# Optimization experiments

Measured on AMD Instinct MI355X. Metric: run time of the kernel, lower is better.

Reference implementation:

```python
import jax, jax.numpy as jnp
import numpy as np

B, T, DIM, FF, E, TOPK = 2, 2048, 1024, 4096, 8, 2


def setup_inputs() -> dict:
    key = jax.random.key(0)
    k0, k1, k2, k3 = jax.random.split(key, 4)
    x = jax.random.normal(k0, (B, T, DIM), jnp.float32)
    # router weight [E, D] (nn.Linear(dim, num_experts, bias=False))
    Wr = jax.random.normal(k1, (E, DIM), jnp.float32) * (DIM ** -0.5)
    # per-expert FFN weights, stacked: W1 [E, D, FF], W2 [E, FF, D]
    W1 = jax.random.normal(k2, (E, DIM, FF), jnp.float32) * (DIM ** -0.5)
    W2 = jax.random.normal(k3, (E, FF, DIM), jnp.float32) * (FF ** -0.5)
    return {"x": x, "Wr": Wr, "W1": W1, "W2": W2}


def reference(x, Wr, W1, W2):
    """MoEFeedForward.forward, world_size=1, STANDARD implementation.

    Math: per token, top_k experts by router logits, softmax over the top_k
    logits (fp32), y = sum_k w_k * FFN_{e_k}(x). The torch code realizes this
    via sort/permute + per-expert variable-size GEMM + weighted index_add;
    the scatter-add result is identical to the dense masked form below,
    which is the jit-friendly (static-shape) expression.
    """
    Bn, Tn, D = x.shape
    num_experts = Wr.shape[0]
    xf = x.reshape(-1, D)                      # [N, D], N = B*T
    N = xf.shape[0]

    logits = xf @ Wr.T                         # [N, E]
    topw, topi = jax.lax.top_k(logits, TOPK)   # [N, K]
    topw = jax.nn.softmax(topw.astype(jnp.float32), axis=-1).astype(x.dtype)

    # combine weight for each (token, expert): [N, E] (0 if not routed)
    combine = jnp.zeros((N, num_experts), x.dtype)
    combine = combine.at[jnp.arange(N)[:, None], topi].add(topw)

    out = jnp.zeros_like(xf)
    for e in range(num_experts):               # fixed small loop over experts
        h = jax.nn.gelu(xf @ W1[e], approximate=False)  # exact GELU (nn.GELU)
        out = out + combine[:, e:e + 1] * (h @ W2[e])
    return out.reshape(Bn, Tn, D)
```

## Files before the change

kernel.cpp:

```cpp
#include <hip/hip_runtime.h>
#include <hip/hip_bf16.h>
#include <hip/hip_fp16.h>

#define NTOK 4096
#define DIM 1024
#define FF 4096
#define NE 8
#define NSLOT 8192

typedef _Float16 half8 __attribute__((ext_vector_type(8)));
typedef _Float16 half4 __attribute__((ext_vector_type(4)));
typedef float floatx4 __attribute__((ext_vector_type(4)));

__device__ __forceinline__ float gelu_exact(float x) {
    return 0.5f * x * (1.0f + erff(x * 0.70710678118654752f));
}

__device__ __forceinline__ void gl_lds16(const void* g, void* l) {
    __builtin_amdgcn_global_load_lds(
        (const __attribute__((address_space(1))) void*)g,
        (__attribute__((address_space(3))) void*)l, 16, 0, 0);
}

__global__ __launch_bounds__(256) void k_convert_x(const float* __restrict__ x,
                                                   _Float16* __restrict__ xh) {
    int i = (blockIdx.x * 256 + threadIdx.x) * 8;
    float4 a = *(const float4*)(x + i);
    float4 b = *(const float4*)(x + i + 4);
    half8 h;
    h[0] = (_Float16)a.x; h[1] = (_Float16)a.y; h[2] = (_Float16)a.z; h[3] = (_Float16)a.w;
    h[4] = (_Float16)b.x; h[5] = (_Float16)b.y; h[6] = (_Float16)b.z; h[7] = (_Float16)b.w;
    *(half8*)(xh + i) = h;
}

__global__ __launch_bounds__(256) void k_transpose(const float* __restrict__ src,
                                                   _Float16* __restrict__ dst,
                                                   int R, int C) {
    __shared__ float t[64][65];
    int e = blockIdx.z;
    const float* s = src + (size_t)e * R * C;
    _Float16* d = dst + (size_t)e * C * R;
    int r0 = blockIdx.y * 64, c0 = blockIdx.x * 64;
    int tid = threadIdx.x;
    int rr = tid >> 4, cc = (tid & 15) * 4;
#pragma unroll
    for (int i = 0; i < 4; ++i) {
        float4 v = *(const float4*)(s + (size_t)(r0 + rr + i * 16) * C + c0 + cc);
        t[rr + i * 16][cc] = v.x; t[rr + i * 16][cc + 1] = v.y;
        t[rr + i * 16][cc + 2] = v.z; t[rr + i * 16][cc + 3] = v.w;
    }
    __syncthreads();
    int f = tid >> 3, ch = tid & 7;
#pragma unroll
    for (int j = 0; j < 2; ++j) {
        int fr = f + j * 32;
        half8 v;
#pragma unroll
        for (int u = 0; u < 8; ++u) v[u] = (_Float16)t[ch * 8 + u][fr];
        *(half8*)(d + (size_t)(c0 + fr) * R + r0 + ch * 8) = v;
    }
}

__global__ __launch_bounds__(256) void k_router(const float* __restrict__ x,
                                                const float* __restrict__ Wr,
                                                int* __restrict__ counts,
                                                int* __restrict__ tok_e,
                                                float* __restrict__ tok_w,
                                                int* __restrict__ tok_pos) {
    __shared__ float wr[NE * DIM];
    int tid = threadIdx.x;
    for (int i = tid; i < NE * DIM / 4; i += 256)
        ((float4*)wr)[i] = ((const float4*)Wr)[i];
    __syncthreads();

    int w = tid >> 6, lane = tid & 63;
    int t = blockIdx.x * 4 + w;

    float acc[NE] = {};
    for (int j = 0; j < DIM / 64; ++j) {
        float xv = x[t * DIM + j * 64 + lane];
#pragma unroll
        for (int e = 0; e < NE; ++e)
            acc[e] += xv * wr[e * DIM + j * 64 + lane];
    }
#pragma unroll
    for (int e = 0; e < NE; ++e) {
#pragma unroll
        for (int s = 32; s; s >>= 1) acc[e] += __shfl_xor(acc[e], s, 64);
    }
    if (lane == 0) {
        int b0 = 0; float m0 = acc[0];
#pragma unroll
        for (int e = 1; e < NE; ++e) { if (acc[e] > m0) { m0 = acc[e]; b0 = e; } }
        int b1 = -1; float m1 = -1e30f;
#pragma unroll
        for (int e = 0; e < NE; ++e) { if (e != b0 && acc[e] > m1) { m1 = acc[e]; b1 = e; } }
        float z = __expf(m1 - m0);
        float zz = 1.0f / (1.0f + z);
        int p0 = atomicAdd(&counts[b0], 1);
        int p1 = atomicAdd(&counts[b1], 1);
        tok_e[2 * t] = b0;  tok_e[2 * t + 1] = b1;
        tok_w[2 * t] = zz;  tok_w[2 * t + 1] = z * zz;
        tok_pos[2 * t] = p0; tok_pos[2 * t + 1] = p1;
    }
}

__global__ void k_prefix(const int* __restrict__ counts, int* __restrict__ offs,
                         int* __restrict__ tmap256, int* __restrict__ tmap128) {
    if (threadIdx.x == 0 && blockIdx.x == 0) {
        int s = 0, n2 = 0, n1 = 0;
        for (int e = 0; e < NE; ++e) {
            offs[e] = s;
            int c = counts[e];
            for (int mt = 0; mt * 256 < c; ++mt) tmap256[1 + n2++] = (e << 16) | mt;
            for (int mt = 0; mt * 128 < c; ++mt) tmap128[1 + n1++] = (e << 16) | mt;
            s += c;
        }
        offs[NE] = s;
        tmap256[0] = n2;
        tmap128[0] = n1;
    }
}

__global__ __launch_bounds__(256) void k_slots(const int* __restrict__ offs,
                                               const int* __restrict__ tok_e,
                                               const int* __restrict__ tok_pos,
                                               int* __restrict__ tok_slot,
                                               int* __restrict__ list_tok) {
    int idx = blockIdx.x * 256 + threadIdx.x;
    if (idx < NSLOT) {
        int e = tok_e[idx];
        int slot = offs[e] + tok_pos[idx];
        tok_slot[idx] = slot;
        list_tok[slot] = idx >> 1;
    }
}

template<int K, int NOUT, int KSPAN, bool GATHER, bool GELU>
__global__ __launch_bounds__(512, 2) void k_ffn256(
    const _Float16* __restrict__ Abase,
    const _Float16* __restrict__ Wbase,
    const int* __restrict__ tmap,
    const int* __restrict__ counts,
    const int* __restrict__ offs,
    const int* __restrict__ list_tok,
    _Float16* __restrict__ Out) {

    int nt_m = tmap[0];
    if ((int)blockIdx.x >= nt_m) return;
    int ent = tmap[1 + blockIdx.x];
    int e = ent >> 16, mt = ent & 0xffff;
    int base = offs[e] + mt * 256;
    int valid = counts[e] - mt * 256;
    int f0 = blockIdx.y * 256;
    int kbase = blockIdx.z * KSPAN;
    Out += (size_t)blockIdx.z * ((size_t)NSLOT * NOUT);

    __shared__ _Float16 lds[65536];

    int tid = threadIdx.x;
    int wid = tid >> 6, lane = tid & 63;

    const char* AB = (const char*)Abase;
    const char* WB = (const char*)(Wbase + (size_t)e * NOUT * K);

    size_t aoff[4]; unsigned boff[4];
#pragma unroll
    for (int i = 0; i < 4; ++i) {
        int g = i * 512 + tid;
        int r = g >> 3;
        int c = (g & 7) ^ (r & 7);
        int rr = (r < valid) ? r : (valid - 1);
        unsigned arow = GATHER ? (unsigned)list_tok[base + rr] : (unsigned)(base + rr);
        aoff[i] = (size_t)arow * (K * 2) + c * 16 + (size_t)kbase * 2;
        boff[i] = (unsigned)(f0 + r) * (unsigned)(K * 2) + c * 16 + (unsigned)kbase * 2;
    }

    floatx4 acc[8][4];
#pragma unroll
    for (int m = 0; m < 8; ++m)
#pragma unroll
        for (int n = 0; n < 4; ++n) acc[m][n] = (floatx4){0.f, 0.f, 0.f, 0.f};

    int la = lane & 15, lb = lane >> 4;
    int wmb = (wid >> 2) * 128, wnb = (wid & 3) * 64;

#pragma unroll
    for (int i = 0; i < 4; ++i)
        gl_lds16(AB + aoff[i], lds + i * 4096 + wid * 512);
#pragma unroll
    for (int i = 0; i < 4; ++i)
        gl_lds16(WB + boff[i], lds + 32768 + i * 4096 + wid * 512);
    asm volatile("s_waitcnt vmcnt(0)" ::: "memory");
    __builtin_amdgcn_s_barrier();
    __builtin_amdgcn_sched_barrier(0);

    constexpr int NT = KSPAN / 64;
#pragma unroll 2
    for (int t = 0; t < NT; ++t) {
        int cur = t & 1;
        if (t + 1 < NT) {
            size_t adv = (size_t)(t + 1) * 128;
            _Float16* Ad = lds + (cur ^ 1) * 16384;
            _Float16* Bd = lds + 32768 + (cur ^ 1) * 16384;
#pragma unroll
            for (int i = 0; i < 4; ++i)
                gl_lds16(AB + aoff[i] + adv, Ad + i * 4096 + wid * 512);
#pragma unroll
            for (int i = 0; i < 4; ++i)
                gl_lds16(WB + boff[i] + adv, Bd + i * 4096 + wid * 512);
        }
        const _Float16* Ac = lds + cur * 16384;
        const _Float16* Bc = lds + 32768 + cur * 16384;
#pragma unroll
        for (int kk = 0; kk < 2; ++kk) {
            half8 af[8], bf[4];
#pragma unroll
            for (int n = 0; n < 4; ++n) {
                int row = wnb + n * 16 + la;
                int c = kk * 4 + lb;
                bf[n] = *(const half8*)(Bc + row * 64 + ((c ^ (row & 7)) * 8));
            }
#pragma unroll
            for (int m = 0; m < 8; ++m) {
                int row = wmb + m * 16 + la;
                int c = kk * 4 + lb;
                af[m] = *(const half8*)(Ac + row * 64 + ((c ^ (row & 7)) * 8));
            }
#pragma unroll
            for (int m = 0; m < 8; ++m)
#pragma unroll
                for (int n = 0; n < 4; ++n)
                    acc[m][n] = __builtin_amdgcn_mfma_f32_16x16x32_f16(af[m], bf[n], acc[m][n], 0, 0, 0);
        }
        __builtin_amdgcn_sched_barrier(0);
        asm volatile("s_waitcnt vmcnt(0)" ::: "memory");
        __builtin_amdgcn_s_barrier();
        __builtin_amdgcn_sched_barrier(0);
    }

    _Float16* tw = lds + wid * 4096;
#pragma unroll
    for (int ps = 0; ps < 2; ++ps) {
#pragma unroll
        for (int fi = 0; fi < 4; ++fi)
#pragma unroll
            for (int nf = 0; nf < 4; ++nf) {
                floatx4 v = acc[ps * 4 + fi][nf];
#pragma unroll
                for (int i2 = 0; i2 < 4; ++i2) {
                    float fv = v[i2];
                    if (GELU) fv = gelu_exact(fv);
                    tw[(fi * 16 + lb * 4 + i2) * 64 + nf * 16 + la] = (_Float16)fv;
                }
            }
        asm volatile("s_waitcnt lgkmcnt(0)" ::: "memory");
        __builtin_amdgcn_sched_barrier(0);
#pragma unroll
        for (int i2 = 0; i2 < 8; ++i2) {
            int gi = i2 * 64 + lane;
            int row = gi >> 3, c8 = gi & 7;
            half8 v = *(const half8*)(tw + gi * 8);
            int trow = wmb + ps * 64 + row;
            if (trow < valid)
                *(half8*)(Out + (size_t)(base + trow) * NOUT + f0 + wnb + c8 * 8) = v;
        }
    }
}

template<int K, int NOUT, bool GATHER, bool GELU>
__global__ __launch_bounds__(256) void k_ffn(
    const _Float16* __restrict__ Abase,
    const _Float16* __restrict__ Wbase,
    const int* __restrict__ tmap,
    const int* __restrict__ counts,
    const int* __restrict__ offs,
    const int* __restrict__ list_tok,
    _Float16* __restrict__ Out) {

    int nt_m = tmap[0];
    if ((int)blockIdx.x >= nt_m) return;
    int ent = tmap[1 + blockIdx.x];
    int e = ent >> 16, mt = ent & 0xffff;
    int base = offs[e] + mt * 128;
    int valid = counts[e] - mt * 128;
    int f0 = blockIdx.y * 128;

    __shared__ _Float16 lds[32768];

    int tid = threadIdx.x;
    int wid = tid >> 6, lane = tid & 63;

    const char* AB = (const char*)Abase;
    const char* WB = (const char*)(Wbase + (size_t)e * NOUT * K);

    size_t aoff[4]; unsigned boff[4];
#pragma unroll
    for (int i = 0; i < 4; ++i) {
        int g = wid * 256 + i * 64 + lane;
        int r = g >> 3;
        int c = (g & 7) ^ (r & 7);
        int rr = (r < valid) ? r : (valid - 1);
        unsigned arow = GATHER ? (unsigned)list_tok[base + rr] : (unsigned)(base + rr);
        aoff[i] = (size_t)arow * (K * 2) + c * 16;
        boff[i] = (unsigned)(f0 + r) * (unsigned)(K * 2) + c * 16;
    }

    floatx4 acc[4][4];
#pragma unroll
    for (int m = 0; m < 4; ++m)
#pragma unroll
        for (int n = 0; n < 4; ++n) acc[m][n] = (floatx4){0.f, 0.f, 0.f, 0.f};

    int la = lane & 15, lb = lane >> 4;
    int wm = (wid >> 1) * 64, wn = (wid & 1) * 64;

#pragma unroll
    for (int i = 0; i < 4; ++i)
        gl_lds16(AB + aoff[i], lds + wid * 2048 + i * 512);
#pragma unroll
    for (int i = 0; i < 4; ++i)
        gl_lds16(WB + boff[i], lds + 16384 + wid * 2048 + i * 512);
    asm volatile("s_waitcnt vmcnt(0)" ::: "memory");
    __builtin_amdgcn_s_barrier();
    __builtin_amdgcn_sched_barrier(0);

    constexpr int NT = K / 64;
#pragma unroll 2
    for (int t = 0; t < NT; ++t) {
        int cur = t & 1;
        if (t + 1 < NT) {
            size_t kadv = (size_t)(t + 1) * 128;
            _Float16* Ad = lds + (cur ^ 1) * 8192;
            _Float16* Bd = lds + 16384 + (cur ^ 1) * 8192;
#pragma unroll
            for (int i = 0; i < 4; ++i)
                gl_lds16(AB + aoff[i] + kadv, Ad + wid * 2048 + i * 512);
#pragma unroll
            for (int i = 0; i < 4; ++i)
                gl_lds16(WB + boff[i] + kadv, Bd + wid * 2048 + i * 512);
        }
        const _Float16* Ac = lds + cur * 8192;
        const _Float16* Bc = lds + 16384 + cur * 8192;
#pragma unroll
        for (int kk = 0; kk < 2; ++kk) {
            half8 af[4], bf[4];
#pragma unroll
            for (int m = 0; m < 4; ++m) {
                int row = wm + m * 16 + la;
                int c = kk * 4 + lb;
                af[m] = *(const half8*)(Ac + row * 64 + ((c ^ (row & 7)) * 8));
            }
#pragma unroll
            for (int n = 0; n < 4; ++n) {
                int row = wn + n * 16 + la;
                int c = kk * 4 + lb;
                bf[n] = *(const half8*)(Bc + row * 64 + ((c ^ (row & 7)) * 8));
            }
#pragma unroll
            for (int m = 0; m < 4; ++m)
#pragma unroll
                for (int n = 0; n < 4; ++n)
                    acc[m][n] = __builtin_amdgcn_mfma_f32_16x16x32_f16(af[m], bf[n], acc[m][n], 0, 0, 0);
        }
        __builtin_amdgcn_sched_barrier(0);
        asm volatile("s_waitcnt vmcnt(0)" ::: "memory");
        __builtin_amdgcn_s_barrier();
        __builtin_amdgcn_sched_barrier(0);
    }

    _Float16* tw = lds + wid * 4096;
#pragma unroll
    for (int m = 0; m < 4; ++m)
#pragma unroll
        for (int n = 0; n < 4; ++n) {
            floatx4 v = acc[m][n];
#pragma unroll
            for (int i = 0; i < 4; ++i) {
                float fv = v[i];
                if (GELU) fv = gelu_exact(fv);
                tw[(m * 16 + lb * 4 + i) * 64 + n * 16 + la] = (_Float16)fv;
            }
        }
    asm volatile("s_waitcnt lgkmcnt(0)" ::: "memory");
    __builtin_amdgcn_sched_barrier(0);
#pragma unroll
    for (int i = 0; i < 8; ++i) {
        int gi = i * 64 + lane;
        int row = gi >> 3, c8 = gi & 7;
        half8 v = *(const half8*)(tw + gi * 8);
        int trow = wm + row;
        if (trow < valid)
            *(half8*)(Out + (size_t)(base + trow) * NOUT + f0 + wn + c8 * 8) = v;
    }
}

__global__ __launch_bounds__(256) void k_combine(const _Float16* __restrict__ yp,
                                                 const int* __restrict__ tok_slot,
                                                 const float* __restrict__ tok_w,
                                                 float* __restrict__ out,
                                                 int nsplit) {
    int t = blockIdx.x;
    int d = threadIdx.x * 4;
    int s0 = tok_slot[2 * t], s1 = tok_slot[2 * t + 1];
    float w0 = tok_w[2 * t], w1 = tok_w[2 * t + 1];
    float4 sum0 = {0.f, 0.f, 0.f, 0.f}, sum1 = {0.f, 0.f, 0.f, 0.f};
    for (int z = 0; z < nsplit; ++z) {
        const _Float16* p = yp + (size_t)z * NSLOT * DIM;
        half4 y0 = *(const half4*)(p + (size_t)s0 * DIM + d);
        half4 y1 = *(const half4*)(p + (size_t)s1 * DIM + d);
        sum0.x += (float)y0[0]; sum0.y += (float)y0[1];
        sum0.z += (float)y0[2]; sum0.w += (float)y0[3];
        sum1.x += (float)y1[0]; sum1.y += (float)y1[1];
        sum1.z += (float)y1[2]; sum1.w += (float)y1[3];
    }
    float4 o;
    o.x = w0 * sum0.x + w1 * sum1.x;
    o.y = w0 * sum0.y + w1 * sum1.y;
    o.z = w0 * sum0.z + w1 * sum1.z;
    o.w = w0 * sum0.w + w1 * sum1.w;
    *(float4*)(out + (size_t)t * DIM + d) = o;
}

extern "C" void kernel_launch(void* const* d_in, const int* in_sizes, int n_in,
                              void* d_out, int out_size, void* d_ws, size_t ws_size,
                              hipStream_t stream) {
    const float* x  = (const float*)d_in[0];
    const float* Wr = (const float*)d_in[1];
    const float* W1 = (const float*)d_in[2];
    const float* W2 = (const float*)d_in[3];
    float* out = (float*)d_out;

    char* ws = (char*)d_ws;
    _Float16* w1t  = (_Float16*)ws;
    _Float16* w2t  = (_Float16*)ws;
    _Float16* xh   = (_Float16*)(ws + 67108864);
    _Float16* hbuf = (_Float16*)(ws + 75497472);
    char* p = ws + 142606336;
    int*   counts   = (int*)p;        p += 1024;
    int*   offs     = (int*)p;        p += 1024;
    int*   tmap256  = (int*)p;        p += 1024;
    int*   tmap128  = (int*)p;        p += 1024;
    int*   tok_e    = (int*)p;        p += NSLOT * 4;
    float* tok_w    = (float*)p;      p += NSLOT * 4;
    int*   tok_pos  = (int*)p;        p += NSLOT * 4;
    int*   tok_slot = (int*)p;        p += NSLOT * 4;
    int*   list_tok = (int*)p;        p += NSLOT * 4;
    const size_t OFF_Y = 142606336 + 196608;
    const size_t SZ_Y  = (size_t)NSLOT * DIM * 2;
    _Float16* yp = (_Float16*)(ws + OFF_Y);

    int nsplit = (ws_size >= OFF_Y + 4 * SZ_Y) ? 4
               : (ws_size >= OFF_Y + 2 * SZ_Y) ? 2 : 1;

    hipMemsetAsync(counts, 0, NE * sizeof(int), stream);
    k_convert_x<<<NTOK * DIM / (256 * 8), 256, 0, stream>>>(x, xh);
    k_router<<<NTOK / 4, 256, 0, stream>>>(x, Wr, counts, tok_e, tok_w, tok_pos);
    k_prefix<<<1, 64, 0, stream>>>(counts, offs, tmap256, tmap128);
    k_slots<<<NSLOT / 256, 256, 0, stream>>>(offs, tok_e, tok_pos, tok_slot, list_tok);

    k_transpose<<<dim3(FF / 64, DIM / 64, NE), 256, 0, stream>>>(W1, w1t, DIM, FF);
    k_ffn256<DIM, FF, DIM, true, true>
        <<<dim3(NSLOT / 256 + NE, FF / 256), 512, 0, stream>>>(
            xh, w1t, tmap256, counts, offs, list_tok, hbuf);
    k_transpose<<<dim3(DIM / 64, FF / 64, NE), 256, 0, stream>>>(W2, w2t, FF, DIM);
    if (nsplit == 4) {
        k_ffn256<FF, DIM, 1024, false, false>
            <<<dim3(NSLOT / 256 + NE, DIM / 256, 4), 512, 0, stream>>>(
                hbuf, w2t, tmap256, counts, offs, list_tok, yp);
    } else if (nsplit == 2) {
        k_ffn256<FF, DIM, 2048, false, false>
            <<<dim3(NSLOT / 256 + NE, DIM / 256, 2), 512, 0, stream>>>(
                hbuf, w2t, tmap256, counts, offs, list_tok, yp);
    } else {
        k_ffn<FF, DIM, false, false>
            <<<dim3(NSLOT / 128 + NE, DIM / 128), 256, 0, stream>>>(
                hbuf, w2t, tmap128, counts, offs, list_tok, yp);
    }
    k_combine<<<NTOK, 256, 0, stream>>>(yp, tok_slot, tok_w, out, nsplit);
}
```

Before: 433.7 us.

## Fuse W2 transpose into FFN1 kernel via interleaved block roles

Adds a fused kernel whose blocks either run a 128-tile FFN1 GEMM or transpose a tile of W2, interleaved 2:7 across a flat grid. The transpose then overlaps with the first GEMM instead of running serially between the two GEMMs. The W2 transpose goes to a separate workspace region and the split-K output reuses the W1 buffer. FFN1 now uses 128x128 tiles with 256 threads instead of 256x256 tiles with 512 threads, which may lower per-block GEMM efficiency. The fused path only runs when the workspace is large enough, and otherwise falls back to a layout without the 4-way split.

```diff
diff --git a/kernel.cpp b/kernel.cpp
--- a/kernel.cpp
+++ b/kernel.cpp
@@ -33,32 +33,39 @@
     *(half8*)(xh + i) = h;
 }
 
+template<typename LdsT>
+__device__ __forceinline__ void transpose_tile(const float* __restrict__ s,
+                                               _Float16* __restrict__ d,
+                                               int R, int C, int r0, int c0,
+                                               LdsT* ldsraw) {
+    float (*t)[65] = (float (*)[65])ldsraw;
+    int tid = threadIdx.x;
+    int rr = tid >> 4, cc = (tid & 15) * 4;
+#pragma unroll
+    for (int i = 0; i < 4; ++i) {
+        float4 v = *(const float4*)(s + (size_t)(r0 + rr + i * 16) * C + c0 + cc);
+        t[rr + i * 16][cc] = v.x; t[rr + i * 16][cc + 1] = v.y;
+        t[rr + i * 16][cc + 2] = v.z; t[rr + i * 16][cc + 3] = v.w;
+    }
+    __syncthreads();
+    int f = tid >> 3, ch = tid & 7;
+#pragma unroll
+    for (int j = 0; j < 2; ++j) {
+        int fr = f + j * 32;
+        half8 v;
+#pragma unroll
+        for (int u = 0; u < 8; ++u) v[u] = (_Float16)t[ch * 8 + u][fr];
+        *(half8*)(d + (size_t)(c0 + fr) * R + r0 + ch * 8) = v;
+    }
+}
+
 __global__ __launch_bounds__(256) void k_transpose(const float* __restrict__ src,
                                                    _Float16* __restrict__ dst,
                                                    int R, int C) {
     __shared__ float t[64][65];
     int e = blockIdx.z;
-    const float* s = src + (size_t)e * R * C;
-    _Float16* d = dst + (size_t)e * C * R;
-    int r0 = blockIdx.y * 64, c0 = blockIdx.x * 64;
-    int tid = threadIdx.x;
-    int rr = tid >> 4, cc = (tid & 15) * 4;
-#pragma unroll
-    for (int i = 0; i < 4; ++i) {
-        float4 v = *(const float4*)(s + (size_t)(r0 + rr + i * 16) * C + c0 + cc);
-        t[rr + i * 16][cc] = v.x; t[rr + i * 16][cc + 1] = v.y;
-        t[rr + i * 16][cc + 2] = v.z; t[rr + i * 16][cc + 3] = v.w;
-    }
-    __syncthreads();
-    int f = tid >> 3, ch = tid & 7;
-#pragma unroll
-    for (int j = 0; j < 2; ++j) {
-        int fr = f + j * 32;
-        half8 v;
-#pragma unroll
-        for (int u = 0; u < 8; ++u) v[u] = (_Float16)t[ch * 8 + u][fr];
-        *(half8*)(d + (size_t)(c0 + fr) * R + r0 + ch * 8) = v;
-    }
+    transpose_tile(src + (size_t)e * R * C, dst + (size_t)e * C * R,
+                   R, C, blockIdx.y * 64, blockIdx.x * 64, &t[0][0]);
 }
 
 __global__ __launch_bounds__(256) void k_router(const float* __restrict__ x,
@@ -136,6 +143,174 @@
     }
 }
 
+template<int K, int NOUT, bool GATHER, bool GELU>
+__device__ __forceinline__ void ffn128_body(
+    const _Float16* __restrict__ Abase,
+    const _Float16* __restrict__ Wbase,
+    const int* __restrict__ counts,
+    const int* __restrict__ offs,
+    const int* __restrict__ list_tok,
+    _Float16* __restrict__ Out,
+    int e, int mt, int f0, _Float16* lds) {
+
+    int base = offs[e] + mt * 128;
+    int valid = counts[e] - mt * 128;
+
+    int tid = threadIdx.x;
+    int wid = tid >> 6, lane = tid & 63;
+
+    const char* AB = (const char*)Abase;
+    const char* WB = (const char*)(Wbase + (size_t)e * NOUT * K);
+
+    size_t aoff[4]; unsigned boff[4];
+#pragma unroll
+    for (int i = 0; i < 4; ++i) {
+        int g = wid * 256 + i * 64 + lane;
+        int r = g >> 3;
+        int c = (g & 7) ^ (r & 7);
+        int rr = (r < valid) ? r : (valid - 1);
+        unsigned arow = GATHER ? (unsigned)list_tok[base + rr] : (unsigned)(base + rr);
+        aoff[i] = (size_t)arow * (K * 2) + c * 16;
+        boff[i] = (unsigned)(f0 + r) * (unsigned)(K * 2) + c * 16;
+    }
+
+    floatx4 acc[4][4];
+#pragma unroll
+    for (int m = 0; m < 4; ++m)
+#pragma unroll
+        for (int n = 0; n < 4; ++n) acc[m][n] = (floatx4){0.f, 0.f, 0.f, 0.f};
+
+    int la = lane & 15, lb = lane >> 4;
+    int wm = (wid >> 1) * 64, wn = (wid & 1) * 64;
+
+#pragma unroll
+    for (int i = 0; i < 4; ++i)
+        gl_lds16(AB + aoff[i], lds + wid * 2048 + i * 512);
+#pragma unroll
+    for (int i = 0; i < 4; ++i)
+        gl_lds16(WB + boff[i], lds + 16384 + wid * 2048 + i * 512);
+    asm volatile("s_waitcnt vmcnt(0)" ::: "memory");
+    __builtin_amdgcn_s_barrier();
+    __builtin_amdgcn_sched_barrier(0);
+
+    constexpr int NT = K / 64;
+#pragma unroll 2
+    for (int t = 0; t < NT; ++t) {
+        int cur = t & 1;
+        if (t + 1 < NT) {
+            size_t kadv = (size_t)(t + 1) * 128;
+            _Float16* Ad = lds + (cur ^ 1) * 8192;
+            _Float16* Bd = lds + 16384 + (cur ^ 1) * 8192;
+#pragma unroll
+            for (int i = 0; i < 4; ++i)
+                gl_lds16(AB + aoff[i] + kadv, Ad + wid * 2048 + i * 512);
+#pragma unroll
+            for (int i = 0; i < 4; ++i)
+                gl_lds16(WB + boff[i] + kadv, Bd + wid * 2048 + i * 512);
+        }
+        const _Float16* Ac = lds + cur * 8192;
+        const _Float16* Bc = lds + 16384 + cur * 8192;
+#pragma unroll
+        for (int kk = 0; kk < 2; ++kk) {
+            half8 af[4], bf[4];
+#pragma unroll
+            for (int m = 0; m < 4; ++m) {
+                int row = wm + m * 16 + la;
+                int c = kk * 4 + lb;
+                af[m] = *(const half8*)(Ac + row * 64 + ((c ^ (row & 7)) * 8));
+            }
+#pragma unroll
+            for (int n = 0; n < 4; ++n) {
+                int row = wn + n * 16 + la;
+                int c = kk * 4 + lb;
+                bf[n] = *(const half8*)(Bc + row * 64 + ((c ^ (row & 7)) * 8));
+            }
+#pragma unroll
+            for (int m = 0; m < 4; ++m)
+#pragma unroll
+                for (int n = 0; n < 4; ++n)
+                    acc[m][n] = __builtin_amdgcn_mfma_f32_16x16x32_f16(af[m], bf[n], acc[m][n], 0, 0, 0);
+        }
+        __builtin_amdgcn_sched_barrier(0);
+        asm volatile("s_waitcnt vmcnt(0)" ::: "memory");
+        __builtin_amdgcn_s_barrier();
+        __builtin_amdgcn_sched_barrier(0);
+    }
+
+    _Float16* tw = lds + wid * 4096;
+#pragma unroll
+    for (int m = 0; m < 4; ++m)
+#pragma unroll
+        for (int n = 0; n < 4; ++n) {
+            floatx4 v = acc[m][n];
+#pragma unroll
+            for (int i = 0; i < 4; ++i) {
+                float fv = v[i];
+                if (GELU) fv = gelu_exact(fv);
+                tw[(m * 16 + lb * 4 + i) * 64 + n * 16 + la] = (_Float16)fv;
+            }
+        }
+    asm volatile("s_waitcnt lgkmcnt(0)" ::: "memory");
+    __builtin_amdgcn_sched_barrier(0);
+#pragma unroll
+    for (int i = 0; i < 8; ++i) {
+        int gi = i * 64 + lane;
+        int row = gi >> 3, c8 = gi & 7;
+        half8 v = *(const half8*)(tw + gi * 8);
+        int trow = wm + row;
+        if (trow < valid)
+            *(half8*)(Out + (size_t)(base + trow) * NOUT + f0 + wn + c8 * 8) = v;
+    }
+}
+
+template<int K, int NOUT, bool GATHER, bool GELU>
+__global__ __launch_bounds__(256) void k_ffn(
+    const _Float16* __restrict__ Abase,
+    const _Float16* __restrict__ Wbase,
+    const int* __restrict__ tmap,
+    const int* __restrict__ counts,
+    const int* __restrict__ offs,
+    const int* __restrict__ list_tok,
+    _Float16* __restrict__ Out) {
+    __shared__ _Float16 lds[32768];
+    int nt_m = tmap[0];
+    if ((int)blockIdx.x >= nt_m) return;
+    int ent = tmap[1 + blockIdx.x];
+    ffn128_body<K, NOUT, GATHER, GELU>(Abase, Wbase, counts, offs, list_tok, Out,
+                                       ent >> 16, ent & 0xffff, blockIdx.y * 128, lds);
+}
+
+__global__ __launch_bounds__(256) void k_ffn1_fused(
+    const _Float16* __restrict__ xh,
+    const _Float16* __restrict__ w1t,
+    const int* __restrict__ tmap,
+    const int* __restrict__ counts,
+    const int* __restrict__ offs,
+    const int* __restrict__ list_tok,
+    _Float16* __restrict__ hbuf,
+    const float* __restrict__ W2,
+    _Float16* __restrict__ w2t) {
+    __shared__ _Float16 lds[32768];
+    int bid = blockIdx.x;
+    int q = bid / 9, r = bid % 9;
+    if (r < 2) {
+        int f = q * 2 + r;
+        int nt_m = tmap[0];
+        int tile = f >> 5;
+        if (tile >= nt_m) return;
+        int ent = tmap[1 + tile];
+        ffn128_body<DIM, FF, true, true>(xh, w1t, counts, offs, list_tok, hbuf,
+                                         ent >> 16, ent & 0xffff, (f & 31) * 128, lds);
+    } else {
+        int t = q * 7 + (r - 2);
+        if (t >= 16 * 64 * NE) return;
+        int e = t >> 10, rem = t & 1023;
+        int cx = rem & 15, ry = rem >> 4;
+        transpose_tile(W2 + (size_t)e * FF * DIM, w2t + (size_t)e * DIM * FF,
+                       FF, DIM, ry * 64, cx * 64, (float*)lds);
+    }
+}
+
 template<int K, int NOUT, int KSPAN, bool GATHER, bool GELU>
 __global__ __launch_bounds__(512, 2) void k_ffn256(
     const _Float16* __restrict__ Abase,
@@ -265,133 +440,6 @@
             if (trow < valid)
                 *(half8*)(Out + (size_t)(base + trow) * NOUT + f0 + wnb + c8 * 8) = v;
         }
-    }
-}
-
-template<int K, int NOUT, bool GATHER, bool GELU>
-__global__ __launch_bounds__(256) void k_ffn(
-    const _Float16* __restrict__ Abase,
-    const _Float16* __restrict__ Wbase,
-    const int* __restrict__ tmap,
-    const int* __restrict__ counts,
-    const int* __restrict__ offs,
-    const int* __restrict__ list_tok,
-    _Float16* __restrict__ Out) {
-
-    int nt_m = tmap[0];
-    if ((int)blockIdx.x >= nt_m) return;
-    int ent = tmap[1 + blockIdx.x];
-    int e = ent >> 16, mt = ent & 0xffff;
-    int base = offs[e] + mt * 128;
-    int valid = counts[e] - mt * 128;
-    int f0 = blockIdx.y * 128;
-
-    __shared__ _Float16 lds[32768];
-
-    int tid = threadIdx.x;
-    int wid = tid >> 6, lane = tid & 63;
-
-    const char* AB = (const char*)Abase;
-    const char* WB = (const char*)(Wbase + (size_t)e * NOUT * K);
-
-    size_t aoff[4]; unsigned boff[4];
-#pragma unroll
-    for (int i = 0; i < 4; ++i) {
-        int g = wid * 256 + i * 64 + lane;
-        int r = g >> 3;
-        int c = (g & 7) ^ (r & 7);
-        int rr = (r < valid) ? r : (valid - 1);
-        unsigned arow = GATHER ? (unsigned)list_tok[base + rr] : (unsigned)(base + rr);
-        aoff[i] = (size_t)arow * (K * 2) + c * 16;
-        boff[i] = (unsigned)(f0 + r) * (unsigned)(K * 2) + c * 16;
-    }
-
-    floatx4 acc[4][4];
-#pragma unroll
-    for (int m = 0; m < 4; ++m)
-#pragma unroll
-        for (int n = 0; n < 4; ++n) acc[m][n] = (floatx4){0.f, 0.f, 0.f, 0.f};
-
-    int la = lane & 15, lb = lane >> 4;
-    int wm = (wid >> 1) * 64, wn = (wid & 1) * 64;
-
-#pragma unroll
-    for (int i = 0; i < 4; ++i)
-        gl_lds16(AB + aoff[i], lds + wid * 2048 + i * 512);
-#pragma unroll
-    for (int i = 0; i < 4; ++i)
-        gl_lds16(WB + boff[i], lds + 16384 + wid * 2048 + i * 512);
-    asm volatile("s_waitcnt vmcnt(0)" ::: "memory");
-    __builtin_amdgcn_s_barrier();
-    __builtin_amdgcn_sched_barrier(0);
-
-    constexpr int NT = K / 64;
-#pragma unroll 2
-    for (int t = 0; t < NT; ++t) {
-        int cur = t & 1;
-        if (t + 1 < NT) {
-            size_t kadv = (size_t)(t + 1) * 128;
-            _Float16* Ad = lds + (cur ^ 1) * 8192;
-            _Float16* Bd = lds + 16384 + (cur ^ 1) * 8192;
-#pragma unroll
-            for (int i = 0; i < 4; ++i)
-                gl_lds16(AB + aoff[i] + kadv, Ad + wid * 2048 + i * 512);
-#pragma unroll
-            for (int i = 0; i < 4; ++i)
-                gl_lds16(WB + boff[i] + kadv, Bd + wid * 2048 + i * 512);
-        }
-        const _Float16* Ac = lds + cur * 8192;
-        const _Float16* Bc = lds + 16384 + cur * 8192;
-#pragma unroll
-        for (int kk = 0; kk < 2; ++kk) {
-            half8 af[4], bf[4];
-#pragma unroll
-            for (int m = 0; m < 4; ++m) {
-                int row = wm + m * 16 + la;
-                int c = kk * 4 + lb;
-                af[m] = *(const half8*)(Ac + row * 64 + ((c ^ (row & 7)) * 8));
-            }
-#pragma unroll
-            for (int n = 0; n < 4; ++n) {
-                int row = wn + n * 16 + la;
-                int c = kk * 4 + lb;
-                bf[n] = *(const half8*)(Bc + row * 64 + ((c ^ (row & 7)) * 8));
-            }
-#pragma unroll
-            for (int m = 0; m < 4; ++m)
-#pragma unroll
-                for (int n = 0; n < 4; ++n)
-                    acc[m][n] = __builtin_amdgcn_mfma_f32_16x16x32_f16(af[m], bf[n], acc[m][n], 0, 0, 0);
-        }
-        __builtin_amdgcn_sched_barrier(0);
-        asm volatile("s_waitcnt vmcnt(0)" ::: "memory");
-        __builtin_amdgcn_s_barrier();
-        __builtin_amdgcn_sched_barrier(0);
-    }
-
-    _Float16* tw = lds + wid * 4096;
-#pragma unroll
-    for (int m = 0; m < 4; ++m)
-#pragma unroll
-        for (int n = 0; n < 4; ++n) {
-            floatx4 v = acc[m][n];
-#pragma unroll
-            for (int i = 0; i < 4; ++i) {
-                float fv = v[i];
-                if (GELU) fv = gelu_exact(fv);
-                tw[(m * 16 + lb * 4 + i) * 64 + n * 16 + la] = (_Float16)fv;
-            }
-        }
-    asm volatile("s_waitcnt lgkmcnt(0)" ::: "memory");
-    __builtin_amdgcn_sched_barrier(0);
-#pragma unroll
-    for (int i = 0; i < 8; ++i) {
-        int gi = i * 64 + lane;
-        int row = gi >> 3, c8 = gi & 7;
-        half8 v = *(const half8*)(tw + gi * 8);
-        int trow = wm + row;
-        if (trow < valid)
-            *(half8*)(Out + (size_t)(base + trow) * NOUT + f0 + wn + c8 * 8) = v;
     }
 }
 
@@ -433,7 +481,6 @@
 
     char* ws = (char*)d_ws;
     _Float16* w1t  = (_Float16*)ws;
-    _Float16* w2t  = (_Float16*)ws;
     _Float16* xh   = (_Float16*)(ws + 67108864);
     _Float16* hbuf = (_Float16*)(ws + 75497472);
     char* p = ws + 142606336;
@@ -446,36 +493,45 @@
     int*   tok_pos  = (int*)p;        p += NSLOT * 4;
     int*   tok_slot = (int*)p;        p += NSLOT * 4;
     int*   list_tok = (int*)p;        p += NSLOT * 4;
-    const size_t OFF_Y = 142606336 + 196608;
+    const size_t OFF_EXT = 142606336 + 196608;
     const size_t SZ_Y  = (size_t)NSLOT * DIM * 2;
-    _Float16* yp = (_Float16*)(ws + OFF_Y);
-
-    int nsplit = (ws_size >= OFF_Y + 4 * SZ_Y) ? 4
-               : (ws_size >= OFF_Y + 2 * SZ_Y) ? 2 : 1;
+    const size_t SZ_WT = (size_t)NE * DIM * FF * 2;
+
+    bool fused = (ws_size >= OFF_EXT + SZ_WT);
 
     hipMemsetAsync(counts, 0, NE * sizeof(int), stream);
     k_convert_x<<<NTOK * DIM / (256 * 8), 256, 0, stream>>>(x, xh);
     k_router<<<NTOK / 4, 256, 0, stream>>>(x, Wr, counts, tok_e, tok_w, tok_pos);
     k_prefix<<<1, 64, 0, stream>>>(counts, offs, tmap256, tmap128);
     k_slots<<<NSLOT / 256, 256, 0, stream>>>(offs, tok_e, tok_pos, tok_slot, list_tok);
-
     k_transpose<<<dim3(FF / 64, DIM / 64, NE), 256, 0, stream>>>(W1, w1t, DIM, FF);
-    k_ffn256<DIM, FF, DIM, true, true>
-        <<<dim3(NSLOT / 256 + NE, FF / 256), 512, 0, stream>>>(
-            xh, w1t, tmap256, counts, offs, list_tok, hbuf);
-    k_transpose<<<dim3(DIM / 64, FF / 64, NE), 256, 0, stream>>>(W2, w2t, FF, DIM);
-    if (nsplit == 4) {
+
+    if (fused) {
+        _Float16* w2t = (_Float16*)(ws + OFF_EXT);
+        _Float16* yp  = (_Float16*)ws;
+        k_ffn1_fused<<<9 * 1171, 256, 0, stream>>>(
+            xh, w1t, tmap128, counts, offs, list_tok, hbuf, W2, w2t);
         k_ffn256<FF, DIM, 1024, false, false>
             <<<dim3(NSLOT / 256 + NE, DIM / 256, 4), 512, 0, stream>>>(
                 hbuf, w2t, tmap256, counts, offs, list_tok, yp);
-    } else if (nsplit == 2) {
-        k_ffn256<FF, DIM, 2048, false, false>
-            <<<dim3(NSLOT / 256 + NE, DIM / 256, 2), 512, 0, stream>>>(
-                hbuf, w2t, tmap256, counts, offs, list_tok, yp);
+        k_combine<<<NTOK, 256, 0, stream>>>(yp, tok_slot, tok_w, out, 4);
     } else {
-        k_ffn<FF, DIM, false, false>
-            <<<dim3(NSLOT / 128 + NE, DIM / 128), 256, 0, stream>>>(
-                hbuf, w2t, tmap128, counts, offs, list_tok, yp);
-    }
-    k_combine<<<NTOK, 256, 0, stream>>>(yp, tok_slot, tok_w, out, nsplit);
-}
+        _Float16* w2t = w1t;
+        _Float16* yp  = (_Float16*)(ws + OFF_EXT);
+        int nsplit = (ws_size >= OFF_EXT + 2 * SZ_Y) ? 2 : 1;
+        k_ffn<DIM, FF, true, true>
+            <<<dim3(NSLOT / 128 + NE, FF / 128), 256, 0, stream>>>(
+                xh, w1t, tmap128, counts, offs, list_tok, hbuf);
+        k_transpose<<<dim3(DIM / 64, FF / 64, NE), 256, 0, stream>>>(W2, w2t, FF, DIM);
+        if (nsplit == 2) {
+            k_ffn256<FF, DIM, 2048, false, false>
+                <<<dim3(NSLOT / 256 + NE, DIM / 256, 2), 512, 0, stream>>>(
+                    hbuf, w2t, tmap256, counts, offs, list_tok, yp);
+        } else {
+            k_ffn<FF, DIM, false, false>
+                <<<dim3(NSLOT / 128 + NE, DIM / 128), 256, 0, stream>>>(
+                    hbuf, w2t, tmap128, counts, offs, list_tok, yp);
+        }
+        k_combine<<<NTOK, 256, 0, stream>>>(yp, tok_slot, tok_w, out, nsplit);
+    }
+}
```

Result: faster. 408.5 us (-5.8%).
